# Performance work log

Hardware: AMD Instinct MI355X
Metric: run time of the kernel (lower is better)

## Reference

```python
import jax, jax.numpy as jnp
import numpy as np

N = 100000
IN_DIM = 512
HID = (256, 256, 128)
NNZ = 3200000
SLOPE = 0.25  # leaky_relu negative slope


def _spmm(rows, cols, vals, X):
    # out[i] = sum_{e: rows[e]==i} vals[e] * X[cols[e]]  -> sparse [N,N] @ X
    return jax.ops.segment_sum(vals[:, None] * X[cols], rows, num_segments=N)


def setup_inputs() -> dict:
    key = jax.random.key(0)
    ks = jax.random.split(key, 10)
    x = jax.random.normal(ks[0], (N, IN_DIM), dtype=jnp.float32)
    adj_rows = jax.random.randint(ks[1], (NNZ,), 0, N, dtype=jnp.int32)
    adj_cols = jax.random.randint(ks[2], (NNZ,), 0, N, dtype=jnp.int32)
    adj_vals = jax.random.uniform(ks[3], (NNZ,), dtype=jnp.float32)
    # xavier_normal-ish init for weights, zeros for biases
    def xav(k, fan_in, fan_out):
        std = (2.0 / (fan_in + fan_out)) ** 0.5
        return std * jax.random.normal(k, (fan_in, fan_out), dtype=jnp.float32)
    W1 = xav(ks[4], IN_DIM, HID[0]); b1 = jnp.zeros((HID[0],), jnp.float32)
    W2 = xav(ks[5], HID[0], HID[1]); b2 = jnp.zeros((HID[1],), jnp.float32)
    W3 = xav(ks[6], HID[1], HID[2]); b3 = jnp.zeros((HID[2],), jnp.float32)
    return {"x": x, "adj_rows": adj_rows, "adj_cols": adj_cols, "adj_vals": adj_vals,
            "W1": W1, "b1": b1, "W2": W2, "b2": b2, "W3": W3, "b3": b3}


def reference(x, adj_rows, adj_cols, adj_vals, W1, b1, W2, b2, W3, b3):
    # Inference mode: F.dropout with training=False is identity.
    def layer(h, W, b):
        support = h @ W                       # dense GEMM [N, d_out]
        out = _spmm(adj_rows, adj_cols, adj_vals, support) + b
        return jax.nn.leaky_relu(out, SLOPE)
    h = layer(x, W1, b1)
    h = layer(h, W2, b2)
    h = layer(h, W3, b3)
    return h
```

## Files before the change

kernel.cpp:

```cpp
#include <hip/hip_runtime.h>

#define N_NODES 100000
#define NNZ_E   3200000
#define SLOPE   0.25f
#define NBLK_SCAN 98

typedef __attribute__((ext_vector_type(8))) short bf16x8;
typedef __attribute__((ext_vector_type(4))) float f32x4;

__device__ __forceinline__ unsigned short f2b(float f) {
    union { float f; unsigned int u; } c; c.f = f;
    unsigned int u = c.u + 0x7fffu + ((c.u >> 16) & 1u);
    return (unsigned short)(u >> 16);
}
__device__ __forceinline__ float b2f_lo(unsigned int u) {
    union { unsigned int u; float f; } c; c.u = u << 16; return c.f;
}
__device__ __forceinline__ float b2f_hi(unsigned int u) {
    union { unsigned int u; float f; } c; c.u = u & 0xffff0000u; return c.f;
}

__device__ __forceinline__ void load_lds16(const unsigned short* gp, unsigned short* lp) {
    __builtin_amdgcn_global_load_lds(
        (const __attribute__((address_space(1))) void*)gp,
        (__attribute__((address_space(3))) void*)lp, 16, 0, 0);
}

__global__ __launch_bounds__(256) void hist_kernel(const int* __restrict__ rows,
                                                   int* __restrict__ counts) {
    int e = blockIdx.x * blockDim.x + threadIdx.x;
    if (e < NNZ_E) atomicAdd(&counts[rows[e]], 1);
}

__global__ __launch_bounds__(256) void chunk_sum_kernel(const int* __restrict__ counts,
                                                        int* __restrict__ bsum) {
    int b = blockIdx.x, t = threadIdx.x;
    int base = b * 1024 + t * 4;
    int s = 0;
    if (base < N_NODES) {
        int4 v = *(const int4*)&counts[base];
        s = v.x + v.y + v.z + v.w;
    }
    __shared__ int red[256];
    red[t] = s; __syncthreads();
    for (int off = 128; off > 0; off >>= 1) {
        if (t < off) red[t] += red[t + off];
        __syncthreads();
    }
    if (t == 0) bsum[b] = red[0];
}

__global__ __launch_bounds__(128) void bsum_scan_kernel(const int* __restrict__ bsum,
                                                        int* __restrict__ boff) {
    int t = threadIdx.x;
    __shared__ int lds[128];
    int v = (t < NBLK_SCAN) ? bsum[t] : 0;
    lds[t] = v; __syncthreads();
    for (int off = 1; off < 128; off <<= 1) {
        int u = (t >= off) ? lds[t - off] : 0;
        __syncthreads();
        lds[t] += u;
        __syncthreads();
    }
    if (t < NBLK_SCAN) boff[t] = lds[t] - v;
}

__global__ __launch_bounds__(256) void scan_apply_kernel(const int* __restrict__ counts,
                                                         const int* __restrict__ boff,
                                                         int* __restrict__ row_off,
                                                         int* __restrict__ cursor) {
    int b = blockIdx.x, t = threadIdx.x;
    int base = b * 1024 + t * 4;
    int4 v = make_int4(0, 0, 0, 0);
    if (base < N_NODES) v = *(const int4*)&counts[base];
    int s = v.x + v.y + v.z + v.w;
    __shared__ int lds[256];
    lds[t] = s; __syncthreads();
    for (int off = 1; off < 256; off <<= 1) {
        int u = (t >= off) ? lds[t - off] : 0;
        __syncthreads();
        lds[t] += u;
        __syncthreads();
    }
    int run = boff[b] + lds[t] - s;
    if (base < N_NODES) {
        row_off[base + 0] = run; cursor[base + 0] = run; run += v.x;
        row_off[base + 1] = run; cursor[base + 1] = run; run += v.y;
        row_off[base + 2] = run; cursor[base + 2] = run; run += v.z;
        row_off[base + 3] = run; cursor[base + 3] = run; run += v.w;
    }
    if (b == 0 && t == 0) row_off[N_NODES] = NNZ_E;
}

__global__ __launch_bounds__(256) void scatter_kernel(const int* __restrict__ rows,
                                                      const int* __restrict__ cols,
                                                      const float* __restrict__ vals,
                                                      int* __restrict__ cursor,
                                                      int2* __restrict__ epack) {
    int e = blockIdx.x * blockDim.x + threadIdx.x;
    if (e < NNZ_E) {
        int pos = atomicAdd(&cursor[rows[e]], 1);
        epack[pos] = make_int2(cols[e], __float_as_int(vals[e]));
    }
}

__global__ __launch_bounds__(256) void conv_kernel(const float* __restrict__ in,
                                                   unsigned short* __restrict__ out,
                                                   int n4) {
    int i = blockIdx.x * blockDim.x + threadIdx.x;
    if (i < n4) {
        float4 v = *(const float4*)&in[i << 2];
        ushort4 o;
        o.x = f2b(v.x); o.y = f2b(v.y); o.z = f2b(v.z); o.w = f2b(v.w);
        *(ushort4*)&out[i << 2] = o;
    }
}

__global__ __launch_bounds__(256) void wprep_kernel(const float* __restrict__ W,
                                                    unsigned short* __restrict__ Wt,
                                                    int K, int Nc) {
    int idx = blockIdx.x * blockDim.x + threadIdx.x;
    if (idx < K * Nc) {
        int n = idx / K, k = idx - n * K;
        Wt[idx] = f2b(W[(size_t)k * Nc + n]);
    }
}

__global__ __launch_bounds__(256) void gemm_bf16_128(
    const unsigned short* __restrict__ A,
    const unsigned short* __restrict__ Bt,
    unsigned short* __restrict__ C,
    int M, int K, int Nc)
{
    __shared__ __align__(16) unsigned short As[128 * 32];
    __shared__ __align__(16) unsigned short Bs[128 * 32];
    const int t = threadIdx.x;
    const int wave = t >> 6, lane = t & 63;
    const int wm = wave & 1, wn = wave >> 1;
    const int quad = lane >> 4, l16 = lane & 15;
    const int row0 = blockIdx.y * 128, col0 = blockIdx.x * 128;

    f32x4 acc[4][4];
#pragma unroll
    for (int mt = 0; mt < 4; ++mt)
#pragma unroll
        for (int nt = 0; nt < 4; ++nt) acc[mt][nt] = (f32x4){0.f, 0.f, 0.f, 0.f};

    const int sr0 = wave * 16 + (lane >> 2);
    const int sr1 = sr0 + 64;
    const int sc  = (lane & 3) << 3;

    int ra0 = row0 + sr0; if (ra0 > M - 1) ra0 = M - 1;
    int ra1 = row0 + sr1; if (ra1 > M - 1) ra1 = M - 1;
    const int rb0 = col0 + sr0;
    const int rb1 = col0 + sr1;

    for (int k0 = 0; k0 < K; k0 += 32) {
        __syncthreads();
        load_lds16(&A [(size_t)ra0 * K + k0 + sc], &As[(size_t)wave * 512]);
        load_lds16(&A [(size_t)ra1 * K + k0 + sc], &As[(size_t)(wave + 4) * 512]);
        load_lds16(&Bt[(size_t)rb0 * K + k0 + sc], &Bs[(size_t)wave * 512]);
        load_lds16(&Bt[(size_t)rb1 * K + k0 + sc], &Bs[(size_t)(wave + 4) * 512]);
        __syncthreads();

        bf16x8 af[4], bf[4];
#pragma unroll
        for (int mt = 0; mt < 4; ++mt)
            af[mt] = *(const bf16x8*)&As[(wm * 64 + mt * 16 + l16) * 32 + quad * 8];
#pragma unroll
        for (int nt = 0; nt < 4; ++nt)
            bf[nt] = *(const bf16x8*)&Bs[(wn * 64 + nt * 16 + l16) * 32 + quad * 8];
#pragma unroll
        for (int mt = 0; mt < 4; ++mt)
#pragma unroll
            for (int nt = 0; nt < 4; ++nt)
                acc[mt][nt] = __builtin_amdgcn_mfma_f32_16x16x32_bf16(
                    af[mt], bf[nt], acc[mt][nt], 0, 0, 0);
    }

#pragma unroll
    for (int mt = 0; mt < 4; ++mt)
#pragma unroll
        for (int r = 0; r < 4; ++r) {
            int row = row0 + wm * 64 + mt * 16 + quad * 4 + r;
            if (row < M) {
#pragma unroll
                for (int nt = 0; nt < 4; ++nt) {
                    int col = col0 + wn * 64 + nt * 16 + l16;
                    C[(size_t)row * Nc + col] = f2b(acc[mt][nt][r]);
                }
            }
        }
}

__global__ __launch_bounds__(256) void spmm256b_kernel(const int* __restrict__ row_off,
                                                       const int2* __restrict__ ep,
                                                       const unsigned short* __restrict__ sup,
                                                       const float* __restrict__ bias,
                                                       unsigned short* __restrict__ out) {
    int row = (blockIdx.x << 2) + (threadIdx.x >> 6);
    if (row >= N_NODES) return;
    int lane = threadIdx.x & 63;
    int s = row_off[row], e = row_off[row + 1];
    int cb = lane << 2;
    float a0 = 0.f, a1 = 0.f, a2 = 0.f, a3 = 0.f;
    int i = s;
    for (; i + 4 <= e; i += 4) {
        int2 p0 = ep[i], p1 = ep[i + 1], p2 = ep[i + 2], p3 = ep[i + 3];
        float v0 = __int_as_float(p0.y), v1 = __int_as_float(p1.y);
        float v2 = __int_as_float(p2.y), v3 = __int_as_float(p3.y);
        uint2 g0 = *(const uint2*)&sup[((size_t)p0.x << 8) + cb];
        uint2 g1 = *(const uint2*)&sup[((size_t)p1.x << 8) + cb];
        uint2 g2 = *(const uint2*)&sup[((size_t)p2.x << 8) + cb];
        uint2 g3 = *(const uint2*)&sup[((size_t)p3.x << 8) + cb];
        a0 += v0 * b2f_lo(g0.x); a1 += v0 * b2f_hi(g0.x);
        a2 += v0 * b2f_lo(g0.y); a3 += v0 * b2f_hi(g0.y);
        a0 += v1 * b2f_lo(g1.x); a1 += v1 * b2f_hi(g1.x);
        a2 += v1 * b2f_lo(g1.y); a3 += v1 * b2f_hi(g1.y);
        a0 += v2 * b2f_lo(g2.x); a1 += v2 * b2f_hi(g2.x);
        a2 += v2 * b2f_lo(g2.y); a3 += v2 * b2f_hi(g2.y);
        a0 += v3 * b2f_lo(g3.x); a1 += v3 * b2f_hi(g3.x);
        a2 += v3 * b2f_lo(g3.y); a3 += v3 * b2f_hi(g3.y);
    }
    for (; i < e; ++i) {
        int2 p0 = ep[i];
        float v0 = __int_as_float(p0.y);
        uint2 g0 = *(const uint2*)&sup[((size_t)p0.x << 8) + cb];
        a0 += v0 * b2f_lo(g0.x); a1 += v0 * b2f_hi(g0.x);
        a2 += v0 * b2f_lo(g0.y); a3 += v0 * b2f_hi(g0.y);
    }
    float4 bv = *(const float4*)&bias[cb];
    a0 += bv.x; a1 += bv.y; a2 += bv.z; a3 += bv.w;
    a0 = (a0 >= 0.f) ? a0 : SLOPE * a0;
    a1 = (a1 >= 0.f) ? a1 : SLOPE * a1;
    a2 = (a2 >= 0.f) ? a2 : SLOPE * a2;
    a3 = (a3 >= 0.f) ? a3 : SLOPE * a3;
    ushort4 o; o.x = f2b(a0); o.y = f2b(a1); o.z = f2b(a2); o.w = f2b(a3);
    *(ushort4*)&out[((size_t)row << 8) + cb] = o;
}

__global__ __launch_bounds__(256) void spmm128f_kernel(const int* __restrict__ row_off,
                                                       const int2* __restrict__ ep,
                                                       const unsigned short* __restrict__ sup,
                                                       const float* __restrict__ bias,
                                                       float* __restrict__ out) {
    int row = (blockIdx.x << 2) + (threadIdx.x >> 6);
    if (row >= N_NODES) return;
    int lane = threadIdx.x & 63;
    int s = row_off[row], e = row_off[row + 1];
    int cb = lane << 1;
    float a0 = 0.f, a1 = 0.f;
    int i = s;
    for (; i + 4 <= e; i += 4) {
        int2 p0 = ep[i], p1 = ep[i + 1], p2 = ep[i + 2], p3 = ep[i + 3];
        float v0 = __int_as_float(p0.y), v1 = __int_as_float(p1.y);
        float v2 = __int_as_float(p2.y), v3 = __int_as_float(p3.y);
        unsigned int g0 = *(const unsigned int*)&sup[((size_t)p0.x << 7) + cb];
        unsigned int g1 = *(const unsigned int*)&sup[((size_t)p1.x << 7) + cb];
        unsigned int g2 = *(const unsigned int*)&sup[((size_t)p2.x << 7) + cb];
        unsigned int g3 = *(const unsigned int*)&sup[((size_t)p3.x << 7) + cb];
        a0 += v0 * b2f_lo(g0); a1 += v0 * b2f_hi(g0);
        a0 += v1 * b2f_lo(g1); a1 += v1 * b2f_hi(g1);
        a0 += v2 * b2f_lo(g2); a1 += v2 * b2f_hi(g2);
        a0 += v3 * b2f_lo(g3); a1 += v3 * b2f_hi(g3);
    }
    for (; i < e; ++i) {
        int2 p0 = ep[i];
        float v0 = __int_as_float(p0.y);
        unsigned int g0 = *(const unsigned int*)&sup[((size_t)p0.x << 7) + cb];
        a0 += v0 * b2f_lo(g0); a1 += v0 * b2f_hi(g0);
    }
    float2 bv = *(const float2*)&bias[cb];
    a0 += bv.x; a1 += bv.y;
    a0 = (a0 >= 0.f) ? a0 : SLOPE * a0;
    a1 = (a1 >= 0.f) ? a1 : SLOPE * a1;
    *(float2*)&out[((size_t)row << 7) + cb] = make_float2(a0, a1);
}

extern "C" void kernel_launch(void* const* d_in, const int* in_sizes, int n_in,
                              void* d_out, int out_size, void* d_ws, size_t ws_size,
                              hipStream_t stream) {
    const float* x     = (const float*)d_in[0];
    const int*   arows = (const int*)d_in[1];
    const int*   acols = (const int*)d_in[2];
    const float* avals = (const float*)d_in[3];
    const float* W1 = (const float*)d_in[4];
    const float* b1 = (const float*)d_in[5];
    const float* W2 = (const float*)d_in[6];
    const float* b2 = (const float*)d_in[7];
    const float* W3 = (const float*)d_in[8];
    const float* b3 = (const float*)d_in[9];
    float* out = (float*)d_out;

    char* ws = (char*)d_ws;
    unsigned short* xb   = (unsigned short*)(ws);
    unsigned short* bufS = (unsigned short*)(ws + 102400000);
    unsigned short* bufH = (unsigned short*)(ws + 153600000);
    int2*  epack = (int2*)(ws + 204800000);
    int*   roff = (int*)  (ws + 230400000);
    int*   curs = (int*)  (ws + 230800128);
    int*   cnts = (int*)  (ws + 231200128);
    unsigned short* Wt1 = (unsigned short*)(ws + 231200128);
    unsigned short* Wt2 = (unsigned short*)(ws + 230800128);
    unsigned short* Wt3 = (unsigned short*)(ws + 230800128 + 131072);
    int* bsum = (int*)(ws + 153600000);
    int* boff = (int*)(ws + 153600000 + 512);

    hipMemsetAsync(cnts, 0, N_NODES * sizeof(int), stream);
    hist_kernel<<<NNZ_E / 256, 256, 0, stream>>>(arows, cnts);
    chunk_sum_kernel<<<NBLK_SCAN, 256, 0, stream>>>(cnts, bsum);
    bsum_scan_kernel<<<1, 128, 0, stream>>>(bsum, boff);
    scan_apply_kernel<<<NBLK_SCAN, 256, 0, stream>>>(cnts, boff, roff, curs);
    wprep_kernel<<<(512 * 256 + 255) / 256, 256, 0, stream>>>(W1, Wt1, 512, 256);
    scatter_kernel<<<NNZ_E / 256, 256, 0, stream>>>(arows, acols, avals, curs, epack);
    wprep_kernel<<<(256 * 256 + 255) / 256, 256, 0, stream>>>(W2, Wt2, 256, 256);
    wprep_kernel<<<(256 * 128 + 255) / 256, 256, 0, stream>>>(W3, Wt3, 256, 128);

    conv_kernel<<<(100000 * 512 / 4 + 255) / 256, 256, 0, stream>>>(x, xb, 100000 * 512 / 4);

    const int gyc = (N_NODES + 127) / 128;

    gemm_bf16_128<<<dim3(2, gyc), 256, 0, stream>>>(xb, Wt1, bufS, N_NODES, 512, 256);
    spmm256b_kernel<<<25000, 256, 0, stream>>>(roff, epack, bufS, b1, bufH);
    gemm_bf16_128<<<dim3(2, gyc), 256, 0, stream>>>(bufH, Wt2, bufS, N_NODES, 256, 256);
    spmm256b_kernel<<<25000, 256, 0, stream>>>(roff, epack, bufS, b2, bufH);
    gemm_bf16_128<<<dim3(1, gyc), 256, 0, stream>>>(bufH, Wt3, bufS, N_NODES, 256, 128);
    spmm128f_kernel<<<25000, 256, 0, stream>>>(roff, epack, bufS, b3, out);
}
```

Baseline: 1.354 ms.

## Split CSR edge scatter into two-pass bucketed scatter for locality

Replaces the single random scatter of edges into CSR order with two passes. Edges are first scattered into buckets of 16 rows using atomics on a small bucket cursor array, then scattered into their final positions from the bucketed temp arrays. The second pass writes into nearby addresses, which should cut cache-line thrashing on the random writes. In exchange the edge data is read and written an extra time, with two more kernel launches. Temp buffers reuse the xb workspace region before the conversion kernel writes it.

```diff
diff --git a/kernel.cpp b/kernel.cpp
--- a/kernel.cpp
+++ b/kernel.cpp
@@ -4,6 +4,7 @@
 #define NNZ_E   3200000
 #define SLOPE   0.25f
 #define NBLK_SCAN 98
+#define NBUK    6250
 
 typedef __attribute__((ext_vector_type(8))) short bf16x8;
 typedef __attribute__((ext_vector_type(4))) float f32x4;
@@ -92,15 +93,36 @@
     if (b == 0 && t == 0) row_off[N_NODES] = NNZ_E;
 }
 
-__global__ __launch_bounds__(256) void scatter_kernel(const int* __restrict__ rows,
-                                                      const int* __restrict__ cols,
-                                                      const float* __restrict__ vals,
-                                                      int* __restrict__ cursor,
-                                                      int2* __restrict__ epack) {
+__global__ __launch_bounds__(256) void bcur_init_kernel(const int* __restrict__ row_off,
+                                                        int* __restrict__ bcur) {
+    int b = blockIdx.x * blockDim.x + threadIdx.x;
+    if (b < NBUK) bcur[b] = row_off[b * 16];
+}
+
+__global__ __launch_bounds__(256) void bucket_scatter_kernel(const int* __restrict__ rows,
+                                                             const int* __restrict__ cols,
+                                                             const float* __restrict__ vals,
+                                                             int* __restrict__ bcur,
+                                                             int2* __restrict__ tmprc,
+                                                             float* __restrict__ tmpv) {
     int e = blockIdx.x * blockDim.x + threadIdx.x;
     if (e < NNZ_E) {
-        int pos = atomicAdd(&cursor[rows[e]], 1);
-        epack[pos] = make_int2(cols[e], __float_as_int(vals[e]));
+        int r = rows[e];
+        int pos = atomicAdd(&bcur[r >> 4], 1);
+        tmprc[pos] = make_int2(r, cols[e]);
+        tmpv[pos]  = vals[e];
+    }
+}
+
+__global__ __launch_bounds__(256) void final_scatter_kernel(const int2* __restrict__ tmprc,
+                                                            const float* __restrict__ tmpv,
+                                                            int* __restrict__ cursor,
+                                                            int2* __restrict__ epack) {
+    int i = blockIdx.x * blockDim.x + threadIdx.x;
+    if (i < NNZ_E) {
+        int2 rc = tmprc[i];
+        int pos = atomicAdd(&cursor[rc.x], 1);
+        epack[pos] = make_int2(rc.y, __float_as_int(tmpv[i]));
     }
 }
 
@@ -303,8 +325,11 @@
     unsigned short* Wt1 = (unsigned short*)(ws + 231200128);
     unsigned short* Wt2 = (unsigned short*)(ws + 230800128);
     unsigned short* Wt3 = (unsigned short*)(ws + 230800128 + 131072);
+    int2*  tmprc = (int2*)(ws);
+    float* tmpv  = (float*)(ws + 25600000);
     int* bsum = (int*)(ws + 153600000);
     int* boff = (int*)(ws + 153600000 + 512);
+    int* bcur = (int*)(ws + 153600000 + 1024);
 
     hipMemsetAsync(cnts, 0, N_NODES * sizeof(int), stream);
     hist_kernel<<<NNZ_E / 256, 256, 0, stream>>>(arows, cnts);
@@ -312,7 +337,9 @@
     bsum_scan_kernel<<<1, 128, 0, stream>>>(bsum, boff);
     scan_apply_kernel<<<NBLK_SCAN, 256, 0, stream>>>(cnts, boff, roff, curs);
     wprep_kernel<<<(512 * 256 + 255) / 256, 256, 0, stream>>>(W1, Wt1, 512, 256);
-    scatter_kernel<<<NNZ_E / 256, 256, 0, stream>>>(arows, acols, avals, curs, epack);
+    bcur_init_kernel<<<(NBUK + 255) / 256, 256, 0, stream>>>(roff, bcur);
+    bucket_scatter_kernel<<<NNZ_E / 256, 256, 0, stream>>>(arows, acols, avals, bcur, tmprc, tmpv);
+    final_scatter_kernel<<<NNZ_E / 256, 256, 0, stream>>>(tmprc, tmpv, curs, epack);
     wprep_kernel<<<(256 * 256 + 255) / 256, 256, 0, stream>>>(W2, Wt2, 256, 256);
     wprep_kernel<<<(256 * 128 + 255) / 256, 256, 0, stream>>>(W3, Wt3, 256, 128);
 
```

After: 1.503 ms. 11.0% more time.
